# Optimization experiments

Measured on AMD Instinct MI355X. Metric: run time of the kernel, lower is better.

The kernel has to match this reference:

```python
import jax, jax.numpy as jnp
import numpy as np

D_MODEL, D_K, C_DIM = 1024, 64, 64
B, S = 4, 4096


def setup_inputs() -> dict:
    key = jax.random.key(0)
    ks = jax.random.split(key, 10)
    sc = 1.0 / np.sqrt(D_MODEL)
    return {
        "X": jax.random.normal(ks[0], (B, S, D_MODEL), jnp.float32),
        "cultural_embedding": jax.random.normal(ks[1], (B, C_DIM), jnp.float32),
        "WQ": jax.random.normal(ks[2], (D_MODEL, D_K), jnp.float32) * sc,
        "bQ": jnp.zeros((D_K,), jnp.float32),
        "WK": jax.random.normal(ks[3], (D_MODEL, D_K), jnp.float32) * sc,
        "bK": jnp.zeros((D_K,), jnp.float32),
        "WV": jax.random.normal(ks[4], (D_MODEL, D_K), jnp.float32) * sc,
        "bV": jnp.zeros((D_K,), jnp.float32),
        "WC": jax.random.normal(ks[5], (C_DIM, D_K), jnp.float32) * (1.0 / np.sqrt(C_DIM)),
        "bC": jnp.zeros((D_K,), jnp.float32),
        "lam": jnp.float32(1.0),
    }


def reference(X, cultural_embedding, WQ, bQ, WK, bK, WV, bV, WC, bC, lam):
    # Projections: [B,S,d_k]
    Q = jnp.einsum('bsm,mk->bsk', X, WQ) + bQ
    K = jnp.einsum('bsm,mk->bsk', X, WK) + bK
    V = jnp.einsum('bsm,mk->bsk', X, WV) + bV
    # Cultural projection: [B,d_k]
    c_proj = cultural_embedding @ WC + bC
    # Base attention logits [B,S,S]
    base_logits = jnp.einsum('bqk,bsk->bqs', Q, K) / jnp.sqrt(jnp.float32(D_K))
    # Rank-1 cultural bias per query row, scalar lambda gate
    cultural_bias = lam * jnp.einsum('bsd,bd->bs', Q, c_proj)  # [B,S]
    combined = base_logits + cultural_bias[..., None]
    attn = jax.nn.softmax(combined, axis=-1)
    return jnp.einsum('bqs,bsk->bqk', attn, V)
```

## Files before the change

### kernel.cpp

```cpp
#include <hip/hip_runtime.h>

#define B_  4
#define S_  4096
#define DM  1024
#define DK  64
#define NSPLIT 8
#define KSPAN (S_ / NSPLIT)
#define QT  256

typedef _Float16 half8  __attribute__((ext_vector_type(8)));
typedef _Float16 half4v __attribute__((ext_vector_type(4)));
typedef __fp16   fp16x2 __attribute__((ext_vector_type(2)));
typedef float    floatx4 __attribute__((ext_vector_type(4)));

#define QSCALE 0.18033688011112042f
#define EXP2F(x) __builtin_amdgcn_exp2f(x)

__global__ __launch_bounds__(256) void wt_kernel(
    const float* __restrict__ WQ, const float* __restrict__ WK,
    const float* __restrict__ WV, _Float16* __restrict__ Wt)
{
    const int proj = blockIdx.y;
    const float* W = (proj == 0) ? WQ : (proj == 1) ? WK : WV;
    const int k0 = blockIdx.x * 64;
    const int t = threadIdx.x;
    __shared__ float T[64][68];

    #pragma unroll
    for (int p = 0; p < 4; p++) {
        int c = p * 256 + t;
        int k = c >> 4, n4 = (c & 15) * 4;
        float4 v = *(const float4*)(W + (size_t)(k0 + k) * DK + n4);
        T[k][n4 + 0] = v.x; T[k][n4 + 1] = v.y;
        T[k][n4 + 2] = v.z; T[k][n4 + 3] = v.w;
    }
    __syncthreads();

    const int n = t >> 2, kc = (t & 3) * 16;
    half8 h0, h1;
    #pragma unroll
    for (int j = 0; j < 8; j++) h0[j] = (_Float16)T[kc + j][n];
    #pragma unroll
    for (int j = 0; j < 8; j++) h1[j] = (_Float16)T[kc + 8 + j][n];
    _Float16* dst = Wt + ((size_t)proj * 64 + n) * DM + k0 + kc;
    *(half8*)(dst)     = h0;
    *(half8*)(dst + 8) = h1;
}

__device__ inline half8 cvt8_rte(float4 a, float4 b)
{
    half8 h;
    h[0] = (_Float16)a.x; h[1] = (_Float16)a.y;
    h[2] = (_Float16)a.z; h[3] = (_Float16)a.w;
    h[4] = (_Float16)b.x; h[5] = (_Float16)b.y;
    h[6] = (_Float16)b.z; h[7] = (_Float16)b.w;
    return h;
}

__global__ __launch_bounds__(256) void proj_mfma_kernel(
    const float* __restrict__ X, const _Float16* __restrict__ Wt,
    const float* __restrict__ bQ, const float* __restrict__ bK,
    const float* __restrict__ bV,
    _Float16* __restrict__ Qh, _Float16* __restrict__ Kh,
    _Float16* __restrict__ Vt)
{
    const int r0   = blockIdx.x * 64;
    const int t    = threadIdx.x;
    const int wave = t >> 6, lane = t & 63;
    const int quad = lane >> 4, l15 = lane & 15;

    const float* xrow = X + (size_t)(r0 + wave * 16 + l15) * DM;

    floatx4 acc[3][4];
    #pragma unroll
    for (int p = 0; p < 3; p++)
        #pragma unroll
        for (int nt = 0; nt < 4; nt++)
            acc[p][nt] = (floatx4){0.f, 0.f, 0.f, 0.f};

#define LOADX(dst, k)                                                   \
    {                                                                   \
        const float* p_ = xrow + (k) * 64 + quad * 8;                   \
        dst[0] = *(const float4*)(p_);                                  \
        dst[1] = *(const float4*)(p_ + 4);                              \
        dst[2] = *(const float4*)(p_ + 32);                             \
        dst[3] = *(const float4*)(p_ + 36);                             \
    }

    float4 xA[4], xB[4], xC[4];
    LOADX(xA, 0);
    LOADX(xB, 1);

    #pragma unroll
    for (int kt = 0; kt < DM / 64; kt++) {
        if (kt + 2 < DM / 64) LOADX(xC, kt + 2);

        half8 xa0 = cvt8_rte(xA[0], xA[1]);
        half8 xa1 = cvt8_rte(xA[2], xA[3]);

        #pragma unroll
        for (int pr = 0; pr < 3; pr++) {
            #pragma unroll
            for (int nt = 0; nt < 4; nt++) {
                const _Float16* wp =
                    Wt + ((size_t)pr * 64 + nt * 16 + l15) * DM + kt * 64 + quad * 8;
                half8 bf0 = *(const half8*)(wp);
                half8 bf1 = *(const half8*)(wp + 32);
                floatx4 a = acc[pr][nt];
                a = __builtin_amdgcn_mfma_f32_16x16x32_f16(xa0, bf0, a, 0, 0, 0);
                a = __builtin_amdgcn_mfma_f32_16x16x32_f16(xa1, bf1, a, 0, 0, 0);
                acc[pr][nt] = a;
            }
        }

        #pragma unroll
        for (int j = 0; j < 4; j++) { xA[j] = xB[j]; xB[j] = xC[j]; }
    }
#undef LOADX

    float bqv[4], bkv[4], bvv[4];
    #pragma unroll
    for (int nt = 0; nt < 4; nt++) {
        bqv[nt] = bQ[nt * 16 + l15];
        bkv[nt] = bK[nt * 16 + l15];
        bvv[nt] = bV[nt * 16 + l15];
    }

    const int orow = r0 + wave * 16 + quad * 4;
    const int bidx = r0 >> 12;
    const int s0   = (r0 & (S_ - 1)) + wave * 16 + quad * 4;
    #pragma unroll
    for (int nt = 0; nt < 4; nt++) {
        const int d = nt * 16 + l15;
        #pragma unroll
        for (int i = 0; i < 4; i++) {
            Qh[(size_t)(orow + i) * DK + d] =
                (_Float16)((acc[0][nt][i] + bqv[nt]) * QSCALE);
            Kh[(size_t)(orow + i) * DK + d] =
                (_Float16)(acc[1][nt][i] + bkv[nt]);
        }
        half4v hv;
        #pragma unroll
        for (int i = 0; i < 4; i++)
            hv[i] = (_Float16)(acc[2][nt][i] + bvv[nt]);
        *(half4v*)(Vt + (size_t)bidx * DK * S_ + (size_t)d * S_ + s0) = hv;
    }
}

__global__ __launch_bounds__(512, 4) void flash_mfma_kernel(
    const _Float16* __restrict__ Qh, const _Float16* __restrict__ Kh,
    const _Float16* __restrict__ Vt, _Float16* __restrict__ Oph,
    float* __restrict__ Lp)
{
    const int b     = blockIdx.y;
    const int q0    = blockIdx.x * QT;
    const int split = blockIdx.z;
    const int kbase = split * KSPAN;
    const int t     = threadIdx.x;
    const int wave  = t >> 6, lane = t & 63;
    const int quad  = lane >> 4, l15 = lane & 15;

    __shared__ __align__(16) _Float16 Ks[2][64 * 72];
    __shared__ __align__(16) _Float16 Vs[2][64 * 72];

    const _Float16* Qb = Qh + ((size_t)b * S_ + q0) * DK;
    const _Float16* Kb = Kh + ((size_t)b * S_ + kbase) * DK;
    const _Float16* Vb = Vt + (size_t)b * DK * S_ + kbase;

    half8 qf0[2], qf1[2];
    #pragma unroll
    for (int mt = 0; mt < 2; mt++) {
        const _Float16* qr = Qb + (size_t)(wave * 32 + mt * 16 + l15) * DK;
        qf0[mt] = *(const half8*)(qr + quad * 8);
        qf1[mt] = *(const half8*)(qr + 32 + quad * 8);
    }

    floatx4 acc[2][4];
    float rs[2];
    #pragma unroll
    for (int mt = 0; mt < 2; mt++) {
        #pragma unroll
        for (int nt = 0; nt < 4; nt++) acc[mt][nt] = (floatx4){0.f,0.f,0.f,0.f};
        rs[mt] = 0.f;
    }

    const int kr   = t >> 3, kcol = (t & 7) * 8;
    const int krP  = (kr & 32) | ((kr & 4) << 2) | ((kr & 24) >> 1) | (kr & 3);
    half8 kreg = *(const half8*)(Kb + (size_t)kr * DK + kcol);
    half8 vreg = *(const half8*)(Vb + (size_t)kr * S_ + kcol);
    *(half8*)&Ks[0][krP * 72 + kcol] = kreg;
    *(half8*)&Vs[0][kr  * 72 + kcol] = vreg;

    const int NT = KSPAN / 64;
    int cur = 0;
    for (int it = 0; it < NT; it++) {
        __syncthreads();

        if (it + 1 < NT) {
            const int kn = (it + 1) * 64;
            kreg = *(const half8*)(Kb + (size_t)(kn + kr) * DK + kcol);
            vreg = *(const half8*)(Vb + (size_t)kr * S_ + kn + kcol);
        }

        floatx4 sc[2][4];
        __builtin_amdgcn_s_setprio(1);
        #pragma unroll
        for (int nt = 0; nt < 4; nt++) {
            half8 kf0 = *(half8*)&Ks[cur][(nt * 16 + l15) * 72 + quad * 8];
            half8 kf1 = *(half8*)&Ks[cur][(nt * 16 + l15) * 72 + 32 + quad * 8];
            #pragma unroll
            for (int mt = 0; mt < 2; mt++) {
                floatx4 z = (floatx4){0.f, 0.f, 0.f, 0.f};
                z = __builtin_amdgcn_mfma_f32_16x16x32_f16(kf0, qf0[mt], z, 0, 0, 0);
                z = __builtin_amdgcn_mfma_f32_16x16x32_f16(kf1, qf1[mt], z, 0, 0, 0);
                sc[mt][nt] = z;
            }
        }
        __builtin_amdgcn_s_setprio(0);

        half8 pf0[2], pf1[2];
        #pragma unroll
        for (int mt = 0; mt < 2; mt++) {
            float pe[4][4];
            #pragma unroll
            for (int nt = 0; nt < 4; nt++)
                #pragma unroll
                for (int i = 0; i < 4; i++) {
                    pe[nt][i] = EXP2F(sc[mt][nt][i]);
                    rs[mt] += pe[nt][i];
                }
            fp16x2 c0 = __builtin_amdgcn_cvt_pkrtz(pe[0][0], pe[0][1]);
            fp16x2 c1 = __builtin_amdgcn_cvt_pkrtz(pe[0][2], pe[0][3]);
            fp16x2 c2 = __builtin_amdgcn_cvt_pkrtz(pe[1][0], pe[1][1]);
            fp16x2 c3 = __builtin_amdgcn_cvt_pkrtz(pe[1][2], pe[1][3]);
            pf0[mt] = (half8){(_Float16)c0[0], (_Float16)c0[1],
                              (_Float16)c1[0], (_Float16)c1[1],
                              (_Float16)c2[0], (_Float16)c2[1],
                              (_Float16)c3[0], (_Float16)c3[1]};
            fp16x2 c4 = __builtin_amdgcn_cvt_pkrtz(pe[2][0], pe[2][1]);
            fp16x2 c5 = __builtin_amdgcn_cvt_pkrtz(pe[2][2], pe[2][3]);
            fp16x2 c6 = __builtin_amdgcn_cvt_pkrtz(pe[3][0], pe[3][1]);
            fp16x2 c7 = __builtin_amdgcn_cvt_pkrtz(pe[3][2], pe[3][3]);
            pf1[mt] = (half8){(_Float16)c4[0], (_Float16)c4[1],
                              (_Float16)c5[0], (_Float16)c5[1],
                              (_Float16)c6[0], (_Float16)c6[1],
                              (_Float16)c7[0], (_Float16)c7[1]};
        }

        __builtin_amdgcn_s_setprio(1);
        #pragma unroll
        for (int nt = 0; nt < 4; nt++) {
            half8 vf0 = *(half8*)&Vs[cur][(nt * 16 + l15) * 72 + quad * 8];
            half8 vf1 = *(half8*)&Vs[cur][(nt * 16 + l15) * 72 + 32 + quad * 8];
            #pragma unroll
            for (int mt = 0; mt < 2; mt++) {
                floatx4 a = acc[mt][nt];
                a = __builtin_amdgcn_mfma_f32_16x16x32_f16(vf0, pf0[mt], a, 0, 0, 0);
                a = __builtin_amdgcn_mfma_f32_16x16x32_f16(vf1, pf1[mt], a, 0, 0, 0);
                acc[mt][nt] = a;
            }
        }
        __builtin_amdgcn_s_setprio(0);

        if (it + 1 < NT) {
            *(half8*)&Ks[cur ^ 1][krP * 72 + kcol] = kreg;
            *(half8*)&Vs[cur ^ 1][kr  * 72 + kcol] = vreg;
        }
        cur ^= 1;
    }

    const size_t prow = (size_t)split * B_ * S_ + (size_t)b * S_ + q0;
    #pragma unroll
    for (int mt = 0; mt < 2; mt++) {
        float r = rs[mt];
        r += __shfl_xor(r, 16, 64);
        r += __shfl_xor(r, 32, 64);
        const float inv = 1.0f / r;
        const size_t orow = prow + wave * 32 + mt * 16 + l15;
        #pragma unroll
        for (int nt = 0; nt < 4; nt++) {
            half4v hv;
            #pragma unroll
            for (int i = 0; i < 4; i++)
                hv[i] = (_Float16)(acc[mt][nt][i] * inv);
            *(half4v*)(Oph + orow * DK + nt * 16 + quad * 4) = hv;
        }
        if (quad == 0)
            Lp[orow] = r;
    }
}

__global__ __launch_bounds__(256) void combine_kernel(
    const _Float16* __restrict__ Oph, const float* __restrict__ Lp,
    float* __restrict__ O)
{
    const int r  = blockIdx.x * 16 + (threadIdx.x >> 4);
    const int d4 = (threadIdx.x & 15) * 4;
    const int NR = B_ * S_;

    float lw[NSPLIT], lsum = 0.f;
    #pragma unroll
    for (int s = 0; s < NSPLIT; s++) {
        lw[s] = Lp[(size_t)s * NR + r];
        lsum += lw[s];
    }
    const float inv = 1.0f / lsum;

    float o[4] = {0.f, 0.f, 0.f, 0.f};
    #pragma unroll
    for (int s = 0; s < NSPLIT; s++) {
        half4v h = *(const half4v*)(Oph + ((size_t)s * NR + r) * DK + d4);
        const float w = lw[s];
        #pragma unroll
        for (int j = 0; j < 4; j++) o[j] += w * (float)h[j];
    }
    float4 out;
    out.x = o[0] * inv; out.y = o[1] * inv;
    out.z = o[2] * inv; out.w = o[3] * inv;
    *(float4*)(O + (size_t)r * DK + d4) = out;
}

extern "C" void kernel_launch(void* const* d_in, const int* in_sizes, int n_in,
                              void* d_out, int out_size, void* d_ws, size_t ws_size,
                              hipStream_t stream)
{
    const float* X  = (const float*)d_in[0];
    const float* WQ = (const float*)d_in[2];
    const float* bQ = (const float*)d_in[3];
    const float* WK = (const float*)d_in[4];
    const float* bK = (const float*)d_in[5];
    const float* WV = (const float*)d_in[6];
    const float* bV = (const float*)d_in[7];

    char* ws = (char*)d_ws;
    _Float16* Qh  = (_Float16*)ws;  ws += (size_t)B_ * S_ * DK * 2;
    _Float16* Kh  = (_Float16*)ws;  ws += (size_t)B_ * S_ * DK * 2;
    _Float16* Vt  = (_Float16*)ws;  ws += (size_t)B_ * S_ * DK * 2;
    _Float16* Wt  = (_Float16*)ws;  ws += (size_t)3 * 64 * DM * 2;
    _Float16* Oph = (_Float16*)ws;  ws += (size_t)NSPLIT * B_ * S_ * DK * 2;
    float* Lp     = (float*)ws;

    wt_kernel<<<dim3(DM / 64, 3), 256, 0, stream>>>(WQ, WK, WV, Wt);

    proj_mfma_kernel<<<dim3((B_ * S_) / 64), 256, 0, stream>>>(
        X, Wt, bQ, bK, bV, Qh, Kh, Vt);

    flash_mfma_kernel<<<dim3(S_ / QT, B_, NSPLIT), 512, 0, stream>>>(
        Qh, Kh, Vt, Oph, Lp);

    combine_kernel<<<dim3((B_ * S_) / 16), 256, 0, stream>>>(
        Oph, Lp, (float*)d_out);
}
```

Before: 189.0 us.

## Stage X and W tiles in LDS with double buffering in projection kernel

The projection kernel now loads 64-column K-slices of X (converted to fp16) and all three weight matrices into double-buffered shared memory, with global prefetch of the next slice overlapping the MFMAs. Block size doubles to 512 threads, so 8 waves split the 192 output columns into two halves. Before, each wave read the weights straight from global/L2. The aim is to cut redundant global weight traffic and improve load coalescing, at the cost of a barrier per K step and about 36KB of LDS per block.

```diff
diff --git a/kernel.cpp b/kernel.cpp
--- a/kernel.cpp
+++ b/kernel.cpp
@@ -57,7 +57,7 @@
     return h;
 }
 
-__global__ __launch_bounds__(256) void proj_mfma_kernel(
+__global__ __launch_bounds__(512) void proj_mfma_kernel(
     const float* __restrict__ X, const _Float16* __restrict__ Wt,
     const float* __restrict__ bQ, const float* __restrict__ bK,
     const float* __restrict__ bV,
@@ -68,82 +68,114 @@
     const int t    = threadIdx.x;
     const int wave = t >> 6, lane = t & 63;
     const int quad = lane >> 4, l15 = lane & 15;
-
-    const float* xrow = X + (size_t)(r0 + wave * 16 + l15) * DM;
-
-    floatx4 acc[3][4];
+    const int mt   = wave >> 1, nh = wave & 1;
+
+    __shared__ __align__(16) _Float16 Xs[2][64 * 72];
+    __shared__ __align__(16) _Float16 Ws[2][192 * 72];
+
+    const int xr = t >> 3, xc = (t & 7) * 8;
+    const float* xsrc = X + (size_t)(r0 + xr) * DM + xc;
+    int wrow[3], wcol[3];
+    #pragma unroll
+    for (int p = 0; p < 3; p++) {
+        int c = p * 512 + t;
+        wrow[p] = c >> 3; wcol[p] = (c & 7) * 8;
+    }
+
+    floatx4 acc[6];
+    #pragma unroll
+    for (int j = 0; j < 6; j++) acc[j] = (floatx4){0.f, 0.f, 0.f, 0.f};
+
+    float4 xa4 = *(const float4*)(xsrc);
+    float4 xb4 = *(const float4*)(xsrc + 4);
+    half8 wr[3];
     #pragma unroll
     for (int p = 0; p < 3; p++)
-        #pragma unroll
-        for (int nt = 0; nt < 4; nt++)
-            acc[p][nt] = (floatx4){0.f, 0.f, 0.f, 0.f};
-
-#define LOADX(dst, k)                                                   \
-    {                                                                   \
-        const float* p_ = xrow + (k) * 64 + quad * 8;                   \
-        dst[0] = *(const float4*)(p_);                                  \
-        dst[1] = *(const float4*)(p_ + 4);                              \
-        dst[2] = *(const float4*)(p_ + 32);                             \
-        dst[3] = *(const float4*)(p_ + 36);                             \
-    }
-
-    float4 xA[4], xB[4], xC[4];
-    LOADX(xA, 0);
-    LOADX(xB, 1);
-
+        wr[p] = *(const half8*)(Wt + (size_t)wrow[p] * DM + wcol[p]);
+    *(half8*)&Xs[0][xr * 72 + xc] = cvt8_rte(xa4, xb4);
+    #pragma unroll
+    for (int p = 0; p < 3; p++)
+        *(half8*)&Ws[0][wrow[p] * 72 + wcol[p]] = wr[p];
+
+    int cur = 0;
     #pragma unroll
     for (int kt = 0; kt < DM / 64; kt++) {
-        if (kt + 2 < DM / 64) LOADX(xC, kt + 2);
-
-        half8 xa0 = cvt8_rte(xA[0], xA[1]);
-        half8 xa1 = cvt8_rte(xA[2], xA[3]);
-
-        #pragma unroll
-        for (int pr = 0; pr < 3; pr++) {
-            #pragma unroll
-            for (int nt = 0; nt < 4; nt++) {
-                const _Float16* wp =
-                    Wt + ((size_t)pr * 64 + nt * 16 + l15) * DM + kt * 64 + quad * 8;
-                half8 bf0 = *(const half8*)(wp);
-                half8 bf1 = *(const half8*)(wp + 32);
-                floatx4 a = acc[pr][nt];
-                a = __builtin_amdgcn_mfma_f32_16x16x32_f16(xa0, bf0, a, 0, 0, 0);
-                a = __builtin_amdgcn_mfma_f32_16x16x32_f16(xa1, bf1, a, 0, 0, 0);
-                acc[pr][nt] = a;
-            }
-        }
-
-        #pragma unroll
-        for (int j = 0; j < 4; j++) { xA[j] = xB[j]; xB[j] = xC[j]; }
-    }
-#undef LOADX
-
-    float bqv[4], bkv[4], bvv[4];
-    #pragma unroll
-    for (int nt = 0; nt < 4; nt++) {
-        bqv[nt] = bQ[nt * 16 + l15];
-        bkv[nt] = bK[nt * 16 + l15];
-        bvv[nt] = bV[nt * 16 + l15];
-    }
-
-    const int orow = r0 + wave * 16 + quad * 4;
+        __syncthreads();
+
+        if (kt + 1 < DM / 64) {
+            const int kn = (kt + 1) * 64;
+            xa4 = *(const float4*)(xsrc + kn);
+            xb4 = *(const float4*)(xsrc + kn + 4);
+            #pragma unroll
+            for (int p = 0; p < 3; p++)
+                wr[p] = *(const half8*)(Wt + (size_t)wrow[p] * DM + kn + wcol[p]);
+        }
+
+        half8 xa0 = *(half8*)&Xs[cur][(mt * 16 + l15) * 72 + quad * 8];
+        half8 xa1 = *(half8*)&Xs[cur][(mt * 16 + l15) * 72 + 32 + quad * 8];
+        #pragma unroll
+        for (int j = 0; j < 6; j++) {
+            const int wn = (nh * 6 + j) * 16 + l15;
+            half8 bf0 = *(half8*)&Ws[cur][wn * 72 + quad * 8];
+            half8 bf1 = *(half8*)&Ws[cur][wn * 72 + 32 + quad * 8];
+            floatx4 a = acc[j];
+            a = __builtin_amdgcn_mfma_f32_16x16x32_f16(xa0, bf0, a, 0, 0, 0);
+            a = __builtin_amdgcn_mfma_f32_16x16x32_f16(xa1, bf1, a, 0, 0, 0);
+            acc[j] = a;
+        }
+
+        if (kt + 1 < DM / 64) {
+            *(half8*)&Xs[cur ^ 1][xr * 72 + xc] = cvt8_rte(xa4, xb4);
+            #pragma unroll
+            for (int p = 0; p < 3; p++)
+                *(half8*)&Ws[cur ^ 1][wrow[p] * 72 + wcol[p]] = wr[p];
+        }
+        cur ^= 1;
+    }
+
+    const int orow = r0 + mt * 16 + quad * 4;
     const int bidx = r0 >> 12;
-    const int s0   = (r0 & (S_ - 1)) + wave * 16 + quad * 4;
-    #pragma unroll
-    for (int nt = 0; nt < 4; nt++) {
-        const int d = nt * 16 + l15;
-        #pragma unroll
-        for (int i = 0; i < 4; i++) {
-            Qh[(size_t)(orow + i) * DK + d] =
-                (_Float16)((acc[0][nt][i] + bqv[nt]) * QSCALE);
-            Kh[(size_t)(orow + i) * DK + d] =
-                (_Float16)(acc[1][nt][i] + bkv[nt]);
-        }
-        half4v hv;
-        #pragma unroll
-        for (int i = 0; i < 4; i++)
-            hv[i] = (_Float16)(acc[2][nt][i] + bvv[nt]);
-        *(half4v*)(Vt + (size_t)bidx * DK * S_ + (size_t)d * S_ + s0) = hv;
+    const int s0   = (r0 & (S_ - 1)) + mt * 16 + quad * 4;
+
+    if (nh == 0) {
+        #pragma unroll
+        for (int j = 0; j < 4; j++) {
+            const int d = j * 16 + l15;
+            const float bq = bQ[d];
+            #pragma unroll
+            for (int i = 0; i < 4; i++)
+                Qh[(size_t)(orow + i) * DK + d] =
+                    (_Float16)((acc[j][i] + bq) * QSCALE);
+        }
+        #pragma unroll
+        for (int j = 4; j < 6; j++) {
+            const int d = (j - 4) * 16 + l15;
+            const float bk = bK[d];
+            #pragma unroll
+            for (int i = 0; i < 4; i++)
+                Kh[(size_t)(orow + i) * DK + d] =
+                    (_Float16)(acc[j][i] + bk);
+        }
+    } else {
+        #pragma unroll
+        for (int j = 0; j < 2; j++) {
+            const int d = (2 + j) * 16 + l15;
+            const float bk = bK[d];
+            #pragma unroll
+            for (int i = 0; i < 4; i++)
+                Kh[(size_t)(orow + i) * DK + d] =
+                    (_Float16)(acc[j][i] + bk);
+        }
+        #pragma unroll
+        for (int j = 2; j < 6; j++) {
+            const int d = (j - 2) * 16 + l15;
+            const float bv = bV[d];
+            half4v hv;
+            #pragma unroll
+            for (int i = 0; i < 4; i++)
+                hv[i] = (_Float16)(acc[j][i] + bv);
+            *(half4v*)(Vt + (size_t)bidx * DK * S_ + (size_t)d * S_ + s0) = hv;
+        }
     }
 }
 
@@ -342,7 +374,7 @@
 
     wt_kernel<<<dim3(DM / 64, 3), 256, 0, stream>>>(WQ, WK, WV, Wt);
 
-    proj_mfma_kernel<<<dim3((B_ * S_) / 64), 256, 0, stream>>>(
+    proj_mfma_kernel<<<dim3((B_ * S_) / 64), 512, 0, stream>>>(
         X, Wt, bQ, bK, bV, Qh, Kh, Vt);
 
     flash_mfma_kernel<<<dim3(S_ / QT, B_, NSPLIT), 512, 0, stream>>>(
```

Measured after the change: 153.8 us. -18.7%, faster.
